# Kernel tuning notes

Hardware: AMD Instinct MI355X
Metric: run time of the kernel (lower is better)

## Reference

```python
import jax, jax.numpy as jnp
import numpy as np

EMBED = 1024
FF = 4096
LN_EPS = 1e-5

def _layernorm(x, gamma, beta):
    mu = jnp.mean(x, axis=-1, keepdims=True)
    var = jnp.var(x, axis=-1, keepdims=True)
    return (x - mu) * jax.lax.rsqrt(var + LN_EPS) * gamma + beta

def setup_inputs() -> dict:
    key = jax.random.key(0)
    ks = jax.random.split(key, 16)
    s = 1.0 / np.sqrt(EMBED)
    s2 = 1.0 / np.sqrt(FF)
    return {
        "x": jax.random.normal(ks[0], (8, 2048, EMBED), dtype=jnp.float32),
        "Wq": jax.random.uniform(ks[1], (EMBED, EMBED), jnp.float32, -s, s),
        "bq": jnp.zeros((EMBED,), jnp.float32),
        "Wk": jax.random.uniform(ks[2], (EMBED, EMBED), jnp.float32, -s, s),
        "bk": jnp.zeros((EMBED,), jnp.float32),
        "Wv": jax.random.uniform(ks[3], (EMBED, EMBED), jnp.float32, -s, s),
        "bv": jnp.zeros((EMBED,), jnp.float32),
        "Wo": jax.random.uniform(ks[4], (EMBED, EMBED), jnp.float32, -s, s),
        "bo": jnp.zeros((EMBED,), jnp.float32),
        "g1": jnp.ones((EMBED,), jnp.float32),
        "b1": jnp.zeros((EMBED,), jnp.float32),
        "g2": jnp.ones((EMBED,), jnp.float32),
        "b2": jnp.zeros((EMBED,), jnp.float32),
        "W1": jax.random.uniform(ks[5], (EMBED, FF), jnp.float32, -s, s),
        "bf1": jnp.zeros((FF,), jnp.float32),
        "W2": jax.random.uniform(ks[6], (FF, EMBED), jnp.float32, -s2, s2),
        "bf2": jnp.zeros((EMBED,), jnp.float32),
    }

def reference(x, Wq, bq, Wk, bk, Wv, bv, Wo, bo, g1, b1, g2, b2, W1, bf1, W2, bf2):
    # Single-head attention (heads arg unused in original forward)
    Q = jnp.einsum('bse,ef->bsf', x, Wq) + bq
    K = jnp.einsum('bse,ef->bsf', x, Wk) + bk
    V = jnp.einsum('bse,ef->bsf', x, Wv) + bv
    scale = 1.0 / jnp.sqrt(jnp.float32(EMBED))
    scores = jnp.einsum('bqe,bke->bqk', Q, K) * scale  # [B,S,S]
    attn = jax.nn.softmax(scores, axis=-1)
    attn_out = jnp.einsum('bqk,bke->bqe', attn, V)
    attn_out = jnp.einsum('bse,ef->bsf', attn_out, Wo) + bo
    # dropout is identity in eval mode
    h = _layernorm(x + attn_out, g1, b1)
    ffn = jnp.einsum('bsf,fh->bsh', jax.nn.relu(jnp.einsum('bse,eh->bsh', h, W1) + bf1), W2) + bf2
    return _layernorm(h + ffn, g2, b2)
```

## Files before the change

### kernel.cpp

```cpp
#include <hip/hip_runtime.h>


typedef __attribute__((ext_vector_type(4))) float  f32x4;
typedef __attribute__((ext_vector_type(8))) short  s16x8;
typedef __attribute__((ext_vector_type(4))) short  s16x4;
typedef unsigned short u16;
typedef unsigned int   u32;

__device__ __forceinline__ float bf2f(short s) {
  u32 u = ((u32)(u16)s) << 16;
  float f; __builtin_memcpy(&f, &u, 4); return f;
}
__device__ __forceinline__ short f2bf(float f) {
  u32 u; __builtin_memcpy(&u, &f, 4);
  u32 r = (u + 0x7fffu + ((u >> 16) & 1u)) >> 16;
  return (short)(u16)r;
}

__device__ __forceinline__ void gload16(const void* g, void* l) {
  __builtin_amdgcn_global_load_lds(
      (const __attribute__((address_space(1))) u32*)g,
      (__attribute__((address_space(3))) u32*)l, 16, 0, 0);
}

__device__ __forceinline__ void stage_half(const char* gop, long long ldb,
                                           long long rowbase, int tt, int h,
                                           u16* ldsop, int tid) {
#pragma unroll
  for (int l = 0; l < 2; ++l) {
    const int o   = (l * 512 + tid) * 16;
    const int rih = o >> 7;
    const int scb = (o & 127) ^ ((rih & 7) << 4);
    gload16(gop + (rowbase + h * 128 + rih) * ldb + (long long)tt * 128 + scb,
            (char*)ldsop + h * 16384 + o);
  }
}

#define SABUF(c) (SMEM + (c) * 16384)
#define SBBUF(c) (SMEM + 32768 + (c) * 16384)

#define RD_A(MH) do { _Pragma("unroll") for (int mi = 0; mi < 4; ++mi) { \
    const int row_ = wm * 64 + (MH) * 128 + mi * 16 + lr; \
    const int sw_ = (row_ & 7) << 4; const int rb_ = row_ << 7; \
    _Pragma("unroll") for (int kk = 0; kk < 2; ++kk) \
      af[mi][kk] = *(const s16x8*)(pa + rb_ + (((kk << 6) | (kg << 4)) ^ sw_)); } } while (0)

#define RD_B(NH) do { _Pragma("unroll") for (int nj = 0; nj < 2; ++nj) { \
    const int row_ = wn * 32 + (NH) * 128 + nj * 16 + lr; \
    const int sw_ = (row_ & 7) << 4; const int rb_ = row_ << 7; \
    _Pragma("unroll") for (int kk = 0; kk < 2; ++kk) \
      bf[NH][nj][kk] = *(const s16x8*)(pb + rb_ + (((kk << 6) | (kg << 4)) ^ sw_)); } } while (0)

#define MM(MH, NH) do { _Pragma("unroll") for (int kk = 0; kk < 2; ++kk) \
    _Pragma("unroll") for (int mi = 0; mi < 4; ++mi) \
    _Pragma("unroll") for (int nj = 0; nj < 2; ++nj) \
      acc[(MH) * 4 + mi][(NH) * 2 + nj] = __builtin_amdgcn_mfma_f32_16x16x32_bf16( \
        af[mi][kk], bf[NH][nj][kk], acc[(MH) * 4 + mi][(NH) * 2 + nj], 0, 0, 0); } while (0)

#define PH_SYNC do { __builtin_amdgcn_s_barrier(); \
    asm volatile("s_waitcnt lgkmcnt(0)"); \
    __builtin_amdgcn_sched_barrier(0); } while (0)

template<int MODE>
__global__ __launch_bounds__(512, 2)
void gemm256(const u16* __restrict__ A, const u16* __restrict__ BT,
             u16* __restrict__ C,
             const float* __restrict__ bias0, const float* __restrict__ bias1,
             const float* __restrict__ bias2, const float* __restrict__ linv,
             int M, int N, int K, float scale,
             long long sA, long long sB, long long sC) {
  __shared__ u16 SMEM[65536];

  const int gx = gridDim.x, gy = gridDim.y;
  const int nwg = gx * gy * gridDim.z;
  const int orig = (blockIdx.z * gy + blockIdx.y) * gx + blockIdx.x;
  const int q = nwg >> 3, r8 = nwg & 7;
  const int xcd = orig & 7, pos = orig >> 3;
  const int wg = (xcd < r8 ? xcd * (q + 1) : r8 * (q + 1) + (xcd - r8) * q) + pos;
  const int bz = wg / (gx * gy);
  const int rem = wg % (gx * gy);
  const long long bm = (long long)(rem / gx) * 256;
  const long long bn = (long long)(rem % gx) * 256;

  const char* Ag = (const char*)(A + (long long)bz * sA);
  const char* Bg = (const char*)(BT + (long long)bz * sB);
  u16* Cb = C + (long long)bz * sC;
  const long long ldb = (long long)K * 2;

  const int tid = threadIdx.x;
  const int lane = tid & 63, wid = tid >> 6;
  const int lr = lane & 15, kg = lane >> 4;
  const int wm = wid >> 2, wn = wid & 3;
  const int NT = K >> 6;

  f32x4 acc[8][4] = {};
  s16x8 af[4][2];
  s16x8 bf[2][2][2];

  stage_half(Ag, ldb, bm, 0, 0, SABUF(0), tid);
  stage_half(Bg, ldb, bn, 0, 0, SBBUF(0), tid);
  stage_half(Ag, ldb, bm, 0, 1, SABUF(0), tid);
  stage_half(Bg, ldb, bn, 0, 1, SBBUF(0), tid);
  stage_half(Ag, ldb, bm, 1, 0, SABUF(1), tid);
  stage_half(Bg, ldb, bn, 1, 0, SBBUF(1), tid);
  asm volatile("s_waitcnt vmcnt(4)");
  __builtin_amdgcn_s_barrier();

  for (int T = 0; T < NT; ++T) {
    const int c = T & 1, cn = c ^ 1;
    const char* pa = (const char*)SABUF(c);
    const char* pb = (const char*)SBBUF(c);

    RD_A(0); RD_B(0);
    if (T + 1 < NT) stage_half(Ag, ldb, bm, T + 1, 1, SABUF(cn), tid);
    PH_SYNC;
    __builtin_amdgcn_s_setprio(1); MM(0, 0); __builtin_amdgcn_s_setprio(0);
    __builtin_amdgcn_s_barrier();

    RD_B(1);
    if (T + 1 < NT) stage_half(Bg, ldb, bn, T + 1, 1, SBBUF(cn), tid);
    PH_SYNC;
    __builtin_amdgcn_s_setprio(1); MM(0, 1); __builtin_amdgcn_s_setprio(0);
    __builtin_amdgcn_s_barrier();

    RD_A(1);
    if (T + 2 < NT) stage_half(Ag, ldb, bm, T + 2, 0, SABUF(c), tid);
    PH_SYNC;
    __builtin_amdgcn_s_setprio(1); MM(1, 0); __builtin_amdgcn_s_setprio(0);
    __builtin_amdgcn_s_barrier();

    if (T + 2 < NT) stage_half(Bg, ldb, bn, T + 2, 0, SBBUF(c), tid);
    PH_SYNC;
    __builtin_amdgcn_s_setprio(1); MM(1, 1); __builtin_amdgcn_s_setprio(0);
    if (T + 2 < NT)      { asm volatile("s_waitcnt vmcnt(4)"); }
    else if (T + 1 < NT) { asm volatile("s_waitcnt vmcnt(0)"); }
    __builtin_amdgcn_s_barrier();
  }

  const long long zM = (long long)bz * M;
  u16* obase; long long ldc, bnl;
  const float* bptr = bias0;
  if (MODE == 5) {
    const int sel = (int)(bn >> 10);
    obase = C + (long long)sel * 16777216;
    ldc = 1024; bnl = bn & 1023;
    bptr = (sel == 0 ? bias0 : sel == 1 ? bias1 : bias2);
  } else { obase = Cb; ldc = N; bnl = bn; }

#pragma unroll
  for (int nh = 0; nh < 2; ++nh)
#pragma unroll
    for (int nj = 0; nj < 2; ++nj) {
      const int col = wn * 32 + nh * 128 + nj * 16 + lr;
      float bv = 0.f;
      if (MODE == 1 || MODE == 2 || MODE == 5) bv = bptr[bnl + col];
#pragma unroll
      for (int mh = 0; mh < 2; ++mh)
#pragma unroll
        for (int mi = 0; mi < 4; ++mi) {
          const int row0 = wm * 64 + mh * 128 + mi * 16 + kg * 4;
#pragma unroll
          for (int r = 0; r < 4; ++r) {
            float v = acc[mh * 4 + mi][nh * 2 + nj][r];
            if (MODE == 1 || MODE == 2 || MODE == 5) v = v * scale + bv;
            if (MODE == 2) v = fmaxf(v, 0.f);
            if (MODE == 3) v = __expf(v * scale);
            if (MODE == 4) v = v * linv[zM + bm + row0 + r];
            SMEM[(row0 + r) * 256 + (col ^ (kg << 4))] = (u16)f2bf(v);
          }
        }
    }
  __syncthreads();
#pragma unroll
  for (int i = 0; i < 16; ++i) {
    const int o   = (i * 512 + tid) * 16;
    const int row = o >> 9;
    const int wb  = o & 511;
    const int gs  = (wb >> 4) ^ (((row >> 2) & 3) << 1);
    s16x8 d = *(const s16x8*)((const char*)SMEM + row * 512 + (gs << 4));
    *(s16x8*)((char*)obase + (((long long)bm + row) * ldc + bnl) * 2 + wb) = d;
  }
}

__global__ __launch_bounds__(256) void cast_f32_bf16(const float* __restrict__ in,
                                                     u16* __restrict__ out) {
  long long i = (long long)blockIdx.x * 256 + threadIdx.x;
  f32x4 v = ((const f32x4*)in)[i];
  s16x4 o;
#pragma unroll
  for (int j = 0; j < 4; j++) o[j] = f2bf(v[j]);
  ((s16x4*)out)[i] = o;
}

__global__ __launch_bounds__(256) void transpose_f32_bf16(const float* __restrict__ in,
                                                          u16* __restrict__ out,
                                                          int R, int C) {
  __shared__ float tile[32][33];
  const int tx = threadIdx.x, ty = threadIdx.y;
  const int r0 = blockIdx.y * 32, c0 = blockIdx.x * 32;
#pragma unroll
  for (int i = 0; i < 32; i += 8)
    tile[ty + i][tx] = in[(long long)(r0 + ty + i) * C + (c0 + tx)];
  __syncthreads();
#pragma unroll
  for (int i = 0; i < 32; i += 8)
    out[(long long)(c0 + ty + i) * R + (r0 + tx)] = (u16)f2bf(tile[tx][ty + i]);
}

__global__ __launch_bounds__(256) void transpose_bf16_bf16(const u16* __restrict__ in,
                                                           u16* __restrict__ out,
                                                           int R, int C,
                                                           long long isb, long long osb) {
  __shared__ u16 tile[32][33];
  in  += (long long)blockIdx.z * isb;
  out += (long long)blockIdx.z * osb;
  const int tx = threadIdx.x, ty = threadIdx.y;
  const int r0 = blockIdx.y * 32, c0 = blockIdx.x * 32;
#pragma unroll
  for (int i = 0; i < 32; i += 8)
    tile[ty + i][tx] = in[(long long)(r0 + ty + i) * C + (c0 + tx)];
  __syncthreads();
#pragma unroll
  for (int i = 0; i < 32; i += 8)
    out[(long long)(c0 + ty + i) * R + (r0 + tx)] = tile[tx][ty + i];
}

__global__ __launch_bounds__(256) void rowinv2048(const u16* __restrict__ P,
                                                  float* __restrict__ linv) {
  const long long row = blockIdx.x;
  const u16* p = P + row * 2048;
  const int t = threadIdx.x;
  s16x8 raw = *(const s16x8*)&p[t * 8];
  float s = 0.f;
#pragma unroll
  for (int j = 0; j < 8; j++) s += bf2f(raw[j]);
#pragma unroll
  for (int off = 32; off > 0; off >>= 1) s += __shfl_xor(s, off);
  __shared__ float red[4];
  if ((t & 63) == 0) red[t >> 6] = s;
  __syncthreads();
  if (t == 0) {
    s = (red[0] + red[1]) + (red[2] + red[3]);
    linv[row] = 1.0f / s;
  }
}

__global__ __launch_bounds__(256) void ln_add_f32bf16(const float* __restrict__ x,
                                                      const u16* __restrict__ a,
                                                      const float* __restrict__ g,
                                                      const float* __restrict__ be,
                                                      u16* __restrict__ out) {
  const long long row = blockIdx.x;
  const int t = threadIdx.x;
  f32x4 xv = ((const f32x4*)(x + row * 1024))[t];
  s16x4 av = ((const s16x4*)(a + row * 1024))[t];
  float v[4]; float sum = 0.f, ss = 0.f;
#pragma unroll
  for (int j = 0; j < 4; j++) { v[j] = xv[j] + bf2f(av[j]); sum += v[j]; ss += v[j] * v[j]; }
#pragma unroll
  for (int off = 32; off > 0; off >>= 1) { sum += __shfl_xor(sum, off); ss += __shfl_xor(ss, off); }
  __shared__ float red[8];
  if ((t & 63) == 0) { red[t >> 6] = sum; red[4 + (t >> 6)] = ss; }
  __syncthreads();
  sum = (red[0] + red[1]) + (red[2] + red[3]);
  ss  = (red[4] + red[5]) + (red[6] + red[7]);
  const float mu   = sum * (1.f / 1024.f);
  const float var  = ss * (1.f / 1024.f) - mu * mu;
  const float rstd = rsqrtf(var + 1e-5f);
  s16x4 o;
#pragma unroll
  for (int j = 0; j < 4; j++) {
    const int c = t * 4 + j;
    o[j] = f2bf((v[j] - mu) * rstd * g[c] + be[c]);
  }
  *(s16x4*)&out[row * 1024 + t * 4] = o;
}

__global__ __launch_bounds__(256) void ln_add_bf16bf16(const u16* __restrict__ h,
                                                       const u16* __restrict__ f,
                                                       const float* __restrict__ g,
                                                       const float* __restrict__ be,
                                                       float* __restrict__ out) {
  const long long row = blockIdx.x;
  const int t = threadIdx.x;
  s16x4 hv = ((const s16x4*)(h + row * 1024))[t];
  s16x4 fv = ((const s16x4*)(f + row * 1024))[t];
  float v[4]; float sum = 0.f, ss = 0.f;
#pragma unroll
  for (int j = 0; j < 4; j++) { v[j] = bf2f(hv[j]) + bf2f(fv[j]); sum += v[j]; ss += v[j] * v[j]; }
#pragma unroll
  for (int off = 32; off > 0; off >>= 1) { sum += __shfl_xor(sum, off); ss += __shfl_xor(ss, off); }
  __shared__ float red[8];
  if ((t & 63) == 0) { red[t >> 6] = sum; red[4 + (t >> 6)] = ss; }
  __syncthreads();
  sum = (red[0] + red[1]) + (red[2] + red[3]);
  ss  = (red[4] + red[5]) + (red[6] + red[7]);
  const float mu   = sum * (1.f / 1024.f);
  const float var  = ss * (1.f / 1024.f) - mu * mu;
  const float rstd = rsqrtf(var + 1e-5f);
  f32x4 o;
#pragma unroll
  for (int j = 0; j < 4; j++) {
    const int c = t * 4 + j;
    o[j] = (v[j] - mu) * rstd * g[c] + be[c];
  }
  ((f32x4*)(out + row * 1024))[t] = o;
}

extern "C" void kernel_launch(void* const* d_in, const int* in_sizes, int n_in,
                              void* d_out, int out_size, void* d_ws, size_t ws_size,
                              hipStream_t stream) {
  const float* x   = (const float*)d_in[0];
  const float* Wq  = (const float*)d_in[1];
  const float* bq  = (const float*)d_in[2];
  const float* Wk  = (const float*)d_in[3];
  const float* bk  = (const float*)d_in[4];
  const float* Wv  = (const float*)d_in[5];
  const float* bv  = (const float*)d_in[6];
  const float* Wo  = (const float*)d_in[7];
  const float* bo  = (const float*)d_in[8];
  const float* g1  = (const float*)d_in[9];
  const float* b1  = (const float*)d_in[10];
  const float* g2  = (const float*)d_in[11];
  const float* b2  = (const float*)d_in[12];
  const float* W1  = (const float*)d_in[13];
  const float* bf1 = (const float*)d_in[14];
  const float* W2  = (const float*)d_in[15];
  const float* bf2 = (const float*)d_in[16];
  float* out = (float*)d_out;

  char* ws = (char*)d_ws;
  u16* wsWQT = (u16*)(ws + 0);
  u16* wsWKT = (u16*)(ws + 2097152);
  u16* wsWVT = (u16*)(ws + 4194304);
  u16* wsWOT = (u16*)(ws + 6291456);
  u16* wsW1T = (u16*)(ws + 8388608);
  u16* wsW2T = (u16*)(ws + 16777216);
  u16* wsXB  = (u16*)(ws + 25165824);
  u16* wsQ   = (u16*)(ws + 58720256);
  u16* wsK   = (u16*)(ws + 92274688);
  u16* wsV   = (u16*)(ws + 125829120);
  u16* wsVT  = (u16*)(ws + 159383552);
  u16* wsS   = (u16*)(ws + 192937984);
  u16* wsAO  = wsXB;
  u16* wsAO2 = wsQ;
  u16* wsH   = wsK;
  u16* wsHID = wsV;
  u16* wsFFN = wsXB;
  float* wsLINV = (float*)wsQ;

  const dim3 tb(32, 8, 1);
  const float inv_sqrt_e = 0.03125f;
  const float* nf = nullptr;

  cast_f32_bf16<<<16384, 256, 0, stream>>>(x, wsXB);

  transpose_f32_bf16<<<dim3(32, 32, 1),  tb, 0, stream>>>(Wq, wsWQT, 1024, 1024);
  transpose_f32_bf16<<<dim3(32, 32, 1),  tb, 0, stream>>>(Wk, wsWKT, 1024, 1024);
  transpose_f32_bf16<<<dim3(32, 32, 1),  tb, 0, stream>>>(Wv, wsWVT, 1024, 1024);
  transpose_f32_bf16<<<dim3(32, 32, 1),  tb, 0, stream>>>(Wo, wsWOT, 1024, 1024);
  transpose_f32_bf16<<<dim3(128, 32, 1), tb, 0, stream>>>(W1, wsW1T, 1024, 4096);
  transpose_f32_bf16<<<dim3(32, 128, 1), tb, 0, stream>>>(W2, wsW2T, 4096, 1024);

  gemm256<5><<<dim3(12, 64, 1), 512, 0, stream>>>(wsXB, wsWQT, wsQ, bq, bk, bv, nf,
                                                  16384, 3072, 1024, 1.f, 0, 0, 0);

  transpose_bf16_bf16<<<dim3(32, 64, 8), tb, 0, stream>>>(wsV, wsVT, 2048, 1024, 2048LL * 1024, 1024LL * 2048);

  gemm256<3><<<dim3(8, 8, 8), 512, 0, stream>>>(wsQ, wsK, wsS, nf, nf, nf, nf,
                                                2048, 2048, 1024, inv_sqrt_e,
                                                2048LL * 1024, 2048LL * 1024, 2048LL * 2048);
  rowinv2048<<<16384, 256, 0, stream>>>(wsS, wsLINV);

  gemm256<4><<<dim3(4, 8, 8), 512, 0, stream>>>(wsS, wsVT, wsAO, nf, nf, nf, wsLINV,
                                                2048, 1024, 2048, 1.f,
                                                2048LL * 2048, 1024LL * 2048, 2048LL * 1024);
  gemm256<1><<<dim3(4, 64, 1), 512, 0, stream>>>(wsAO, wsWOT, wsAO2, bo, nf, nf, nf,
                                                 16384, 1024, 1024, 1.f, 0, 0, 0);

  ln_add_f32bf16<<<16384, 256, 0, stream>>>(x, wsAO2, g1, b1, wsH);

  gemm256<2><<<dim3(16, 64, 1), 512, 0, stream>>>(wsH, wsW1T, wsHID, bf1, nf, nf, nf,
                                                  16384, 4096, 1024, 1.f, 0, 0, 0);

  gemm256<1><<<dim3(4, 64, 1), 512, 0, stream>>>(wsHID, wsW2T, wsFFN, bf2, nf, nf, nf,
                                                 16384, 1024, 4096, 1.f, 0, 0, 0);

  ln_add_bf16bf16<<<16384, 256, 0, stream>>>(wsH, wsFFN, g2, b2, out);

  (void)in_sizes; (void)n_in; (void)out_size; (void)ws_size;
}
```

Baseline: 658.7 us.

## Shrink GEMM tile to 256x128 with simple double-buffered K=32 loop

```diff
diff --git a/kernel.cpp b/kernel.cpp
--- a/kernel.cpp
+++ b/kernel.cpp
@@ -23,53 +23,15 @@
       (__attribute__((address_space(3))) u32*)l, 16, 0, 0);
 }
 
-__device__ __forceinline__ void stage_half(const char* gop, long long ldb,
-                                           long long rowbase, int tt, int h,
-                                           u16* ldsop, int tid) {
-#pragma unroll
-  for (int l = 0; l < 2; ++l) {
-    const int o   = (l * 512 + tid) * 16;
-    const int rih = o >> 7;
-    const int scb = (o & 127) ^ ((rih & 7) << 4);
-    gload16(gop + (rowbase + h * 128 + rih) * ldb + (long long)tt * 128 + scb,
-            (char*)ldsop + h * 16384 + o);
-  }
-}
-
-#define SABUF(c) (SMEM + (c) * 16384)
-#define SBBUF(c) (SMEM + 32768 + (c) * 16384)
-
-#define RD_A(MH) do { _Pragma("unroll") for (int mi = 0; mi < 4; ++mi) { \
-    const int row_ = wm * 64 + (MH) * 128 + mi * 16 + lr; \
-    const int sw_ = (row_ & 7) << 4; const int rb_ = row_ << 7; \
-    _Pragma("unroll") for (int kk = 0; kk < 2; ++kk) \
-      af[mi][kk] = *(const s16x8*)(pa + rb_ + (((kk << 6) | (kg << 4)) ^ sw_)); } } while (0)
-
-#define RD_B(NH) do { _Pragma("unroll") for (int nj = 0; nj < 2; ++nj) { \
-    const int row_ = wn * 32 + (NH) * 128 + nj * 16 + lr; \
-    const int sw_ = (row_ & 7) << 4; const int rb_ = row_ << 7; \
-    _Pragma("unroll") for (int kk = 0; kk < 2; ++kk) \
-      bf[NH][nj][kk] = *(const s16x8*)(pb + rb_ + (((kk << 6) | (kg << 4)) ^ sw_)); } } while (0)
-
-#define MM(MH, NH) do { _Pragma("unroll") for (int kk = 0; kk < 2; ++kk) \
-    _Pragma("unroll") for (int mi = 0; mi < 4; ++mi) \
-    _Pragma("unroll") for (int nj = 0; nj < 2; ++nj) \
-      acc[(MH) * 4 + mi][(NH) * 2 + nj] = __builtin_amdgcn_mfma_f32_16x16x32_bf16( \
-        af[mi][kk], bf[NH][nj][kk], acc[(MH) * 4 + mi][(NH) * 2 + nj], 0, 0, 0); } while (0)
-
-#define PH_SYNC do { __builtin_amdgcn_s_barrier(); \
-    asm volatile("s_waitcnt lgkmcnt(0)"); \
-    __builtin_amdgcn_sched_barrier(0); } while (0)
-
 template<int MODE>
-__global__ __launch_bounds__(512, 2)
+__global__ __launch_bounds__(512, 4)
 void gemm256(const u16* __restrict__ A, const u16* __restrict__ BT,
              u16* __restrict__ C,
              const float* __restrict__ bias0, const float* __restrict__ bias1,
              const float* __restrict__ bias2, const float* __restrict__ linv,
              int M, int N, int K, float scale,
              long long sA, long long sB, long long sC) {
-  __shared__ u16 SMEM[65536];
+  __shared__ u16 SMEM[24576];
 
   const int gx = gridDim.x, gy = gridDim.y;
   const int nwg = gx * gy * gridDim.z;
@@ -80,7 +42,7 @@
   const int bz = wg / (gx * gy);
   const int rem = wg % (gx * gy);
   const long long bm = (long long)(rem / gx) * 256;
-  const long long bn = (long long)(rem % gx) * 256;
+  const long long bn = (long long)(rem % gx) * 128;
 
   const char* Ag = (const char*)(A + (long long)bz * sA);
   const char* Bg = (const char*)(BT + (long long)bz * sB);
@@ -90,51 +52,50 @@
   const int tid = threadIdx.x;
   const int lane = tid & 63, wid = tid >> 6;
   const int lr = lane & 15, kg = lane >> 4;
-  const int wm = wid >> 2, wn = wid & 3;
-  const int NT = K >> 6;
-
-  f32x4 acc[8][4] = {};
-  s16x8 af[4][2];
-  s16x8 bf[2][2][2];
-
-  stage_half(Ag, ldb, bm, 0, 0, SABUF(0), tid);
-  stage_half(Bg, ldb, bn, 0, 0, SBBUF(0), tid);
-  stage_half(Ag, ldb, bm, 0, 1, SABUF(0), tid);
-  stage_half(Bg, ldb, bn, 0, 1, SBBUF(0), tid);
-  stage_half(Ag, ldb, bm, 1, 0, SABUF(1), tid);
-  stage_half(Bg, ldb, bn, 1, 0, SBBUF(1), tid);
-  asm volatile("s_waitcnt vmcnt(4)");
-  __builtin_amdgcn_s_barrier();
+  const int wm = wid >> 1, wn = wid & 1;
+  const int NT = K >> 5;
+
+  f32x4 acc[4][4] = {};
+
+  const int oA0 = tid * 16, oA1 = (512 + tid) * 16, oB0 = tid * 16;
+  const long long arow0 = bm + (oA0 >> 6), arow1 = bm + (oA1 >> 6);
+  const long long brow0 = bn + (oB0 >> 6);
+  const int akoff0 = oA0 & 63, akoff1 = oA1 & 63, bkoff0 = oB0 & 63;
+
+#define STAGE(TT, CN) do { \
+    char* sa_ = (char*)(SMEM + (CN) * 8192); \
+    char* sb_ = (char*)(SMEM + 16384 + (CN) * 4096); \
+    const long long kb_ = (long long)(TT) * 64; \
+    gload16(Ag + arow0 * ldb + kb_ + akoff0, sa_ + oA0); \
+    gload16(Ag + arow1 * ldb + kb_ + akoff1, sa_ + oA1); \
+    gload16(Bg + brow0 * ldb + kb_ + bkoff0, sb_ + oB0); \
+  } while (0)
+
+  STAGE(0, 0);
+  __syncthreads();
 
   for (int T = 0; T < NT; ++T) {
     const int c = T & 1, cn = c ^ 1;
-    const char* pa = (const char*)SABUF(c);
-    const char* pb = (const char*)SBBUF(c);
-
-    RD_A(0); RD_B(0);
-    if (T + 1 < NT) stage_half(Ag, ldb, bm, T + 1, 1, SABUF(cn), tid);
-    PH_SYNC;
-    __builtin_amdgcn_s_setprio(1); MM(0, 0); __builtin_amdgcn_s_setprio(0);
-    __builtin_amdgcn_s_barrier();
-
-    RD_B(1);
-    if (T + 1 < NT) stage_half(Bg, ldb, bn, T + 1, 1, SBBUF(cn), tid);
-    PH_SYNC;
-    __builtin_amdgcn_s_setprio(1); MM(0, 1); __builtin_amdgcn_s_setprio(0);
-    __builtin_amdgcn_s_barrier();
-
-    RD_A(1);
-    if (T + 2 < NT) stage_half(Ag, ldb, bm, T + 2, 0, SABUF(c), tid);
-    PH_SYNC;
-    __builtin_amdgcn_s_setprio(1); MM(1, 0); __builtin_amdgcn_s_setprio(0);
-    __builtin_amdgcn_s_barrier();
-
-    if (T + 2 < NT) stage_half(Bg, ldb, bn, T + 2, 0, SBBUF(c), tid);
-    PH_SYNC;
-    __builtin_amdgcn_s_setprio(1); MM(1, 1); __builtin_amdgcn_s_setprio(0);
-    if (T + 2 < NT)      { asm volatile("s_waitcnt vmcnt(4)"); }
-    else if (T + 1 < NT) { asm volatile("s_waitcnt vmcnt(0)"); }
-    __builtin_amdgcn_s_barrier();
+    if (T + 1 < NT) STAGE(T + 1, cn);
+
+    const char* pa = (const char*)(SMEM + c * 8192);
+    const char* pb = (const char*)(SMEM + 16384 + c * 4096);
+    s16x8 af[4], bfr[4];
+#pragma unroll
+    for (int mi = 0; mi < 4; ++mi)
+      af[mi] = *(const s16x8*)(pa + ((wm * 64 + mi * 16 + lr) << 6) + (kg << 4));
+#pragma unroll
+    for (int nj = 0; nj < 4; ++nj)
+      bfr[nj] = *(const s16x8*)(pb + ((wn * 64 + nj * 16 + lr) << 6) + (kg << 4));
+
+    __builtin_amdgcn_s_setprio(1);
+#pragma unroll
+    for (int mi = 0; mi < 4; ++mi)
+#pragma unroll
+      for (int nj = 0; nj < 4; ++nj)
+        acc[mi][nj] = __builtin_amdgcn_mfma_f32_16x16x32_bf16(af[mi], bfr[nj], acc[mi][nj], 0, 0, 0);
+    __builtin_amdgcn_s_setprio(0);
+    __syncthreads();
   }
 
   const long long zM = (long long)bz * M;
@@ -148,38 +109,42 @@
   } else { obase = Cb; ldc = N; bnl = bn; }
 
 #pragma unroll
-  for (int nh = 0; nh < 2; ++nh)
-#pragma unroll
-    for (int nj = 0; nj < 2; ++nj) {
-      const int col = wn * 32 + nh * 128 + nj * 16 + lr;
-      float bv = 0.f;
-      if (MODE == 1 || MODE == 2 || MODE == 5) bv = bptr[bnl + col];
-#pragma unroll
-      for (int mh = 0; mh < 2; ++mh)
+  for (int b = 0; b < 2; ++b) {
+    if ((wm >> 1) == b) {
+      const int rbase = (wm & 1) * 64;
+#pragma unroll
+      for (int nj = 0; nj < 4; ++nj) {
+        const int col = wn * 64 + nj * 16 + lr;
+        float bv = 0.f;
+        if (MODE == 1 || MODE == 2 || MODE == 5) bv = bptr[bnl + col];
 #pragma unroll
         for (int mi = 0; mi < 4; ++mi) {
-          const int row0 = wm * 64 + mh * 128 + mi * 16 + kg * 4;
+          const int r0 = rbase + mi * 16 + kg * 4;
 #pragma unroll
           for (int r = 0; r < 4; ++r) {
-            float v = acc[mh * 4 + mi][nh * 2 + nj][r];
+            float v = acc[mi][nj][r];
             if (MODE == 1 || MODE == 2 || MODE == 5) v = v * scale + bv;
             if (MODE == 2) v = fmaxf(v, 0.f);
             if (MODE == 3) v = __expf(v * scale);
-            if (MODE == 4) v = v * linv[zM + bm + row0 + r];
-            SMEM[(row0 + r) * 256 + (col ^ (kg << 4))] = (u16)f2bf(v);
+            if (MODE == 4) v = v * linv[zM + bm + b * 128 + r0 + r];
+            SMEM[(r0 + r) * 128 + (col ^ (kg << 4))] = (u16)f2bf(v);
           }
         }
+      }
     }
-  __syncthreads();
-#pragma unroll
-  for (int i = 0; i < 16; ++i) {
-    const int o   = (i * 512 + tid) * 16;
-    const int row = o >> 9;
-    const int wb  = o & 511;
-    const int gs  = (wb >> 4) ^ (((row >> 2) & 3) << 1);
-    s16x8 d = *(const s16x8*)((const char*)SMEM + row * 512 + (gs << 4));
-    *(s16x8*)((char*)obase + (((long long)bm + row) * ldc + bnl) * 2 + wb) = d;
-  }
+    __syncthreads();
+#pragma unroll
+    for (int i = 0; i < 4; ++i) {
+      const int o   = (i * 512 + tid) * 16;
+      const int row = o >> 8;
+      const int wb  = o & 255;
+      const int gs  = (wb >> 4) ^ ((((row) >> 2) & 3) << 1);
+      s16x8 d = *(const s16x8*)((const char*)SMEM + row * 256 + (gs << 4));
+      *(s16x8*)((char*)obase + (((long long)bm + b * 128 + row) * ldc + bnl) * 2 + wb) = d;
+    }
+    __syncthreads();
+  }
+#undef STAGE
 }
 
 __global__ __launch_bounds__(256) void cast_f32_bf16(const float* __restrict__ in,
@@ -362,28 +327,28 @@
   transpose_f32_bf16<<<dim3(128, 32, 1), tb, 0, stream>>>(W1, wsW1T, 1024, 4096);
   transpose_f32_bf16<<<dim3(32, 128, 1), tb, 0, stream>>>(W2, wsW2T, 4096, 1024);
 
-  gemm256<5><<<dim3(12, 64, 1), 512, 0, stream>>>(wsXB, wsWQT, wsQ, bq, bk, bv, nf,
+  gemm256<5><<<dim3(24, 64, 1), 512, 0, stream>>>(wsXB, wsWQT, wsQ, bq, bk, bv, nf,
                                                   16384, 3072, 1024, 1.f, 0, 0, 0);
 
   transpose_bf16_bf16<<<dim3(32, 64, 8), tb, 0, stream>>>(wsV, wsVT, 2048, 1024, 2048LL * 1024, 1024LL * 2048);
 
-  gemm256<3><<<dim3(8, 8, 8), 512, 0, stream>>>(wsQ, wsK, wsS, nf, nf, nf, nf,
-                                                2048, 2048, 1024, inv_sqrt_e,
-                                                2048LL * 1024, 2048LL * 1024, 2048LL * 2048);
+  gemm256<3><<<dim3(16, 8, 8), 512, 0, stream>>>(wsQ, wsK, wsS, nf, nf, nf, nf,
+                                                 2048, 2048, 1024, inv_sqrt_e,
+                                                 2048LL * 1024, 2048LL * 1024, 2048LL * 2048);
   rowinv2048<<<16384, 256, 0, stream>>>(wsS, wsLINV);
 
-  gemm256<4><<<dim3(4, 8, 8), 512, 0, stream>>>(wsS, wsVT, wsAO, nf, nf, nf, wsLINV,
+  gemm256<4><<<dim3(8, 8, 8), 512, 0, stream>>>(wsS, wsVT, wsAO, nf, nf, nf, wsLINV,
                                                 2048, 1024, 2048, 1.f,
                                                 2048LL * 2048, 1024LL * 2048, 2048LL * 1024);
-  gemm256<1><<<dim3(4, 64, 1), 512, 0, stream>>>(wsAO, wsWOT, wsAO2, bo, nf, nf, nf,
+  gemm256<1><<<dim3(8, 64, 1), 512, 0, stream>>>(wsAO, wsWOT, wsAO2, bo, nf, nf, nf,
                                                  16384, 1024, 1024, 1.f, 0, 0, 0);
 
   ln_add_f32bf16<<<16384, 256, 0, stream>>>(x, wsAO2, g1, b1, wsH);
 
-  gemm256<2><<<dim3(16, 64, 1), 512, 0, stream>>>(wsH, wsW1T, wsHID, bf1, nf, nf, nf,
+  gemm256<2><<<dim3(32, 64, 1), 512, 0, stream>>>(wsH, wsW1T, wsHID, bf1, nf, nf, nf,
                                                   16384, 4096, 1024, 1.f, 0, 0, 0);
 
-  gemm256<1><<<dim3(4, 64, 1), 512, 0, stream>>>(wsHID, wsW2T, wsFFN, bf2, nf, nf, nf,
+  gemm256<1><<<dim3(8, 64, 1), 512, 0, stream>>>(wsHID, wsW2T, wsFFN, bf2, nf, nf, nf,
                                                  16384, 1024, 4096, 1.f, 0, 0, 0);
 
   ln_add_bf16bf16<<<16384, 256, 0, stream>>>(wsH, wsFFN, g2, b2, out);
```

Result: slower. 689.2 us (+4.6%).
